# Kernel tuning notes

Hardware: AMD Instinct MI355X
Metric: run time of the kernel (lower is better)

## Reference

```python
import jax, jax.numpy as jnp
import numpy as np


def setup_inputs() -> dict:
    key = jax.random.key(0)
    k1, k2, k3 = jax.random.split(key, 3)
    B, C_in, H, W = 32, 128, 64, 64
    C_out, KH, KW = 256, 3, 3
    x = jax.random.normal(k1, (B, C_in, H, W), dtype=jnp.float32)
    # kaiming_normal fan_out scale ~ sqrt(2 / (C_out*KH*KW)); plain normal is fine for a numeric reference
    weight = jax.random.normal(k2, (C_out, C_in, KH, KW), dtype=jnp.float32) * (2.0 / (C_out * KH * KW)) ** 0.5
    fan_in = C_in * KH * KW
    bound = 1.0 / (fan_in ** 0.5)
    bias = jax.random.uniform(k3, (C_out,), dtype=jnp.float32, minval=-bound, maxval=bound)
    return {"x": x, "weight": weight, "bias": bias}


def reference(x, weight, bias):
    # Equivalent of unfold (im2col) + matmul + fold with stride=1, padding=1:
    # a standard 2D convolution in NCHW/OIHW layout.
    out = jax.lax.conv_general_dilated(
        x, weight,
        window_strides=(1, 1),
        padding=((1, 1), (1, 1)),
        dimension_numbers=("NCHW", "OIHW", "NCHW"),
    )
    return out + bias[None, :, None, None]
```

## Files before the change

### kernel.cpp

```cpp
#include <hip/hip_runtime.h>

typedef __attribute__((ext_vector_type(4))) int   v4i;
typedef __attribute__((ext_vector_type(8))) short s8;
typedef __attribute__((ext_vector_type(4))) float f32x4;
typedef __attribute__((ext_vector_type(16))) float f32x16;

#define GLB __attribute__((address_space(1)))
#define LDS_AS __attribute__((address_space(3)))

__device__ __forceinline__ unsigned short f2bf(float f) {
  unsigned u = __builtin_bit_cast(unsigned, f);
  return (unsigned short)((u + 0x7fffu + ((u >> 16) & 1u)) >> 16);
}

__global__ void prep(const float* __restrict__ x, const float* __restrict__ w,
                     unsigned int* __restrict__ xw, unsigned short* __restrict__ ww) {
  int t = threadIdx.x;
  if (blockIdx.x >= 2048) {
    int o = (blockIdx.x - 2048) * 256 + t;
    int tap = o >> 15;
    int c   = (o >> 13) & 3;
    int cog = (o >> 10) & 7;
    int kk  = (o >> 9) & 1;
    int lh  = (o >> 8) & 1;
    int l31 = (o >> 3) & 31;
    int e   = o & 7;
    int co = cog * 32 + l31;
    int ci = c * 32 + kk * 16 + lh * 8 + e;
    ww[o] = f2bf(w[(co * 128 + ci) * 9 + tap]);
    return;
  }
  __shared__ float tile[128][65];
  int bid = blockIdx.x;
  int b = bid >> 6, h = bid & 63;
  {
    int wcol = t & 63, cl = t >> 6;
    const float* src = x + ((size_t)(b * 128) * 64 + h) * 64 + wcol;
#pragma unroll
    for (int j = 0; j < 32; ++j) {
      int ci = j * 4 + cl;
      tile[ci][wcol] = src[(size_t)ci * 4096];
    }
  }
  unsigned int* dst = xw + (size_t)((b * 66 + h + 1) * 66) * 64;
  if (t < 128) {
    int col = (t >> 6) ? 65 : 0;
    dst[(size_t)col * 64 + (t & 63)] = 0u;
  }
  if (h == 0 || h == 63) {
    unsigned int* rb = xw + (size_t)(b * 66 + (h == 0 ? 0 : 65)) * 66 * 64;
    for (int j = t; j < 66 * 64; j += 256) rb[j] = 0u;
  }
  __syncthreads();
  {
    int ci2 = (t & 63) * 2, wl = t >> 6;
#pragma unroll
    for (int j = 0; j < 16; ++j) {
      int wcol = j * 4 + wl;
      unsigned p = (unsigned)f2bf(tile[ci2][wcol]) |
                   ((unsigned)f2bf(tile[ci2 + 1][wcol]) << 16);
      dst[(size_t)(wcol + 1) * 64 + (t & 63)] = p;
    }
  }
}

__global__ __launch_bounds__(256, 3) void conv_mfma(
    const unsigned short* __restrict__ xw, const unsigned short* __restrict__ ww,
    const float* __restrict__ bias, float* __restrict__ out) {
  __shared__ unsigned short Xl[204 * 128];
  const int tid = threadIdx.x;
  const int lane = tid & 63;
  const int l31 = lane & 31, lh = lane >> 5;
  const int mw = tid >> 6;
  int bid = blockIdx.x;
  bid = (bid & 7) * 256 + (bid >> 3);
  const int b = bid >> 6, h0 = bid & 63;
  const unsigned xlb = (unsigned)(unsigned long long)((LDS_AS void*)Xl);

  {
    const char* xbase = (const char*)xw;
#pragma unroll
    for (int it = 0; it < 13; ++it) {
      int s = tid + it * 256;
      if (s < 3264) {
        int q = s >> 4, p = s & 15;
        int u = p ^ (q & 15);
        int rr = q / 68, cc = q - rr * 68;
        if (cc > 65) cc = 65;
        unsigned src = (unsigned)((b * 66 + h0 + rr) * 66 + cc) * 256u + (unsigned)u * 16u;
        __builtin_amdgcn_global_load_lds((const GLB unsigned int*)(xbase + src),
                                         (LDS_AS unsigned int*)&Xl[s * 8], 16, 0, 0);
      }
    }
  }

  f32x16 acc[2][2];
#pragma unroll
  for (int m = 0; m < 2; ++m)
#pragma unroll
    for (int n = 0; n < 2; ++n)
#pragma unroll
      for (int e = 0; e < 16; ++e) acc[m][n][e] = 0.f;

  v4i areg[3][4];
  v4i breg[2][4];
  const unsigned abyte = (unsigned)(mw * 4096 + lane * 16);

  #define SB __builtin_amdgcn_sched_barrier(0)

  #define ALOAD_ASM(slot, step)                                               \
    do {                                                                      \
      unsigned _wo = (unsigned)(step) * 16384u + abyte;                       \
      asm volatile("global_load_dwordx4 %0, %1, %2 offset:0"                  \
                   : "=v"(areg[slot][0]) : "v"(_wo), "s"(ww));                \
      asm volatile("global_load_dwordx4 %0, %1, %2 offset:1024"               \
                   : "=v"(areg[slot][1]) : "v"(_wo), "s"(ww));                \
      asm volatile("global_load_dwordx4 %0, %1, %2 offset:2048"               \
                   : "=v"(areg[slot][2]) : "v"(_wo), "s"(ww));                \
      asm volatile("global_load_dwordx4 %0, %1, %2 offset:3072"               \
                   : "=v"(areg[slot][3]) : "v"(_wo), "s"(ww));                \
    } while (0)

  #define BLOAD_K0(slot, S)                                                   \
    do {                                                                      \
      const int _t = (S) >> 2, _c = (S) & 3;                                  \
      const int _kh = _t / 3, _kw = _t - _kh * 3;                             \
      const int _q0 = _kh * 68 + _kw + l31;                                   \
      const int _xq = (_q0 & 15) ^ lh;                                        \
      unsigned _a0 = xlb + (unsigned)((_q0 << 8) + (((_c * 4) ^ _xq) << 4));  \
      asm volatile("ds_read_b128 %0, %1" : "=v"(breg[slot][0]) : "v"(_a0));   \
      asm volatile("ds_read_b128 %0, %1 offset:8192"                          \
                   : "=v"(breg[slot][1]) : "v"(_a0));                         \
    } while (0)

  #define BLOAD_K1(slot, S)                                                   \
    do {                                                                      \
      const int _t = (S) >> 2, _c = (S) & 3;                                  \
      const int _kh = _t / 3, _kw = _t - _kh * 3;                             \
      const int _q0 = _kh * 68 + _kw + l31;                                   \
      const int _xq = (_q0 & 15) ^ lh;                                        \
      unsigned _a1 = xlb + (unsigned)((_q0 << 8) + (((_c * 4 + 2) ^ _xq) << 4)); \
      asm volatile("ds_read_b128 %0, %1" : "=v"(breg[slot][2]) : "v"(_a1));   \
      asm volatile("ds_read_b128 %0, %1 offset:8192"                          \
                   : "=v"(breg[slot][3]) : "v"(_a1));                         \
    } while (0)

  #define MFMA(d, af, bf) \
    d = __builtin_amdgcn_mfma_f32_32x32x16_bf16(__builtin_bit_cast(s8, af), \
                                                __builtin_bit_cast(s8, bf), d, 0, 0, 0)

  #define KSTEP(S)                                                            \
    do {                                                                      \
      const int _s = (S);                                                     \
      const int _cs = _s % 3, _bs = _s & 1, _ns = (_s + 1) & 1;               \
      if (_s < 35) asm volatile("s_waitcnt vmcnt(4) lgkmcnt(0)" ::: "memory");\
      else         asm volatile("s_waitcnt vmcnt(0) lgkmcnt(0)" ::: "memory");\
      SB;                                                                     \
      MFMA(acc[0][0], areg[_cs][0], breg[_bs][0]);                            \
      MFMA(acc[1][0], areg[_cs][2], breg[_bs][0]);                            \
      SB;                                                                     \
      if (_s < 34) ALOAD_ASM((_s + 2) % 3, _s + 2);                           \
      SB;                                                                     \
      MFMA(acc[0][1], areg[_cs][0], breg[_bs][1]);                            \
      MFMA(acc[1][1], areg[_cs][2], breg[_bs][1]);                            \
      SB;                                                                     \
      if (_s < 35) BLOAD_K0(_ns, _s + 1);                                     \
      SB;                                                                     \
      MFMA(acc[0][0], areg[_cs][1], breg[_bs][2]);                            \
      MFMA(acc[1][0], areg[_cs][3], breg[_bs][2]);                            \
      SB;                                                                     \
      if (_s < 35) BLOAD_K1(_ns, _s + 1);                                     \
      SB;                                                                     \
      MFMA(acc[0][1], areg[_cs][1], breg[_bs][3]);                            \
      MFMA(acc[1][1], areg[_cs][3], breg[_bs][3]);                            \
    } while (0)

  ALOAD_ASM(0, 0);
  ALOAD_ASM(1, 1);
  asm volatile("s_waitcnt vmcnt(8)" ::: "memory");
  SB;
  __builtin_amdgcn_s_barrier();
  BLOAD_K0(0, 0);
  BLOAD_K1(0, 0);

#pragma unroll
  for (int s = 0; s < 36; ++s) KSTEP(s);

#pragma unroll
  for (int m = 0; m < 2; ++m)
#pragma unroll
    for (int rq = 0; rq < 4; ++rq) {
      const int cob = mw * 64 + m * 32 + 8 * rq + 4 * lh;
      const f32x4 bi = *(const f32x4*)(bias + cob);
#pragma unroll
      for (int n = 0; n < 2; ++n) {
        const int wc = n * 32 + l31;
        size_t base = ((size_t)(b * 256 + cob) * 64 + h0) * 64 + wc;
#pragma unroll
        for (int e = 0; e < 4; ++e)
          out[base + (size_t)e * 4096] = acc[m][n][rq * 4 + e] + bi[e];
      }
    }
}

__global__ void conv_naive(const float* __restrict__ x, const float* __restrict__ w,
                           const float* __restrict__ bias, float* __restrict__ out) {
  int i = blockIdx.x * 256 + threadIdx.x;
  int wc = i & 63, h = (i >> 6) & 63, co = (i >> 12) & 255, b = i >> 20;
  float s = bias[co];
  for (int ci = 0; ci < 128; ++ci)
#pragma unroll
    for (int kh = 0; kh < 3; ++kh) {
      int hh = h + kh - 1;
      if ((unsigned)hh >= 64u) continue;
#pragma unroll
      for (int kw = 0; kw < 3; ++kw) {
        int wg = wc + kw - 1;
        if ((unsigned)wg >= 64u) continue;
        s += x[((b * 128 + ci) * 64 + hh) * 64 + wg] *
             w[((co * 128 + ci) * 3 + kh) * 3 + kw];
      }
    }
  out[i] = s;
}

extern "C" void kernel_launch(void* const* d_in, const int* in_sizes, int n_in,
                              void* d_out, int out_size, void* d_ws, size_t ws_size,
                              hipStream_t stream) {
  const float* x    = (const float*)d_in[0];
  const float* w    = (const float*)d_in[1];
  const float* bias = (const float*)d_in[2];
  float* out = (float*)d_out;

  const size_t X_OFF  = 1ull << 20;
  const size_t XBYTES = 32ull * 66 * 66 * 128 * 2;
  const size_t NEED   = X_OFF + XBYTES;

  if (ws_size >= NEED) {
    unsigned short* ww = (unsigned short*)d_ws;
    unsigned short* xq = (unsigned short*)((char*)d_ws + X_OFF);
    hipLaunchKernelGGL(prep, dim3(3200), dim3(256), 0, stream, x, w,
                       (unsigned int*)xq, ww);
    hipLaunchKernelGGL(conv_mfma, dim3(2048), dim3(256), 0, stream, xq, ww, bias, out);
  } else {
    hipLaunchKernelGGL(conv_naive, dim3(131072), dim3(256), 0, stream, x, w, bias, out);
  }
}
```

Before: 102.7 us.

## Compute two output rows per block to reuse weight fragments across rows

Each block now produces two output rows instead of one, staging four input rows in LDS and doubling the accumulators. Every weight fragment loaded from global memory feeds MFMAs for both rows, which halves weight traffic and the grid size. The K-step pipeline is reorganised into double-buffered A loads with grouped MFMA bursts. The cost is higher register and LDS use, which lowers occupancy from three to two blocks per CU, and fewer blocks to spread across CUs.

Measured after the change: 102.4 us. Within noise of the previous version (-0.3%).

```diff
diff --git a/kernel.cpp b/kernel.cpp
--- a/kernel.cpp
+++ b/kernel.cpp
@@ -64,29 +64,28 @@
   }
 }
 
-__global__ __launch_bounds__(256, 3) void conv_mfma(
+__global__ __launch_bounds__(256, 2) void conv_mfma(
     const unsigned short* __restrict__ xw, const unsigned short* __restrict__ ww,
     const float* __restrict__ bias, float* __restrict__ out) {
-  __shared__ unsigned short Xl[204 * 128];
+  __shared__ unsigned short Xl[264 * 128];
   const int tid = threadIdx.x;
   const int lane = tid & 63;
   const int l31 = lane & 31, lh = lane >> 5;
   const int mw = tid >> 6;
   int bid = blockIdx.x;
-  bid = (bid & 7) * 256 + (bid >> 3);
-  const int b = bid >> 6, h0 = bid & 63;
+  bid = (bid & 7) * 128 + (bid >> 3);
+  const int b = bid >> 5, h0 = (bid & 31) << 1;
   const unsigned xlb = (unsigned)(unsigned long long)((LDS_AS void*)Xl);
 
   {
     const char* xbase = (const char*)xw;
 #pragma unroll
-    for (int it = 0; it < 13; ++it) {
+    for (int it = 0; it < 17; ++it) {
       int s = tid + it * 256;
-      if (s < 3264) {
+      if (s < 4224) {
         int q = s >> 4, p = s & 15;
         int u = p ^ (q & 15);
-        int rr = q / 68, cc = q - rr * 68;
-        if (cc > 65) cc = 65;
+        int rr = q / 66, cc = q - rr * 66;
         unsigned src = (unsigned)((b * 66 + h0 + rr) * 66 + cc) * 256u + (unsigned)u * 16u;
         __builtin_amdgcn_global_load_lds((const GLB unsigned int*)(xbase + src),
                                          (LDS_AS unsigned int*)&Xl[s * 8], 16, 0, 0);
@@ -94,16 +93,17 @@
     }
   }
 
-  f32x16 acc[2][2];
+  f32x16 acc[2][4];
 #pragma unroll
   for (int m = 0; m < 2; ++m)
 #pragma unroll
-    for (int n = 0; n < 2; ++n)
+    for (int n = 0; n < 4; ++n)
 #pragma unroll
       for (int e = 0; e < 16; ++e) acc[m][n][e] = 0.f;
 
-  v4i areg[3][4];
+  v4i areg[2][4];
   v4i breg[2][4];
+  v4i bregB[4];
   const unsigned abyte = (unsigned)(mw * 4096 + lane * 16);
 
   #define SB __builtin_amdgcn_sched_barrier(0)
@@ -121,28 +121,36 @@
                    : "=v"(areg[slot][3]) : "v"(_wo), "s"(ww));                \
     } while (0)
 
-  #define BLOAD_K0(slot, S)                                                   \
+  #define BLOAD01(slot, S)                                                    \
     do {                                                                      \
       const int _t = (S) >> 2, _c = (S) & 3;                                  \
       const int _kh = _t / 3, _kw = _t - _kh * 3;                             \
-      const int _q0 = _kh * 68 + _kw + l31;                                   \
-      const int _xq = (_q0 & 15) ^ lh;                                        \
-      unsigned _a0 = xlb + (unsigned)((_q0 << 8) + (((_c * 4) ^ _xq) << 4));  \
+      const int _q = _kh * 66 + _kw + l31;                                    \
+      const int _x = (_q & 15) ^ lh;                                          \
+      unsigned _a0 = xlb + (unsigned)((_q << 8) + (((_c * 4) ^ _x) << 4));    \
+      unsigned _a1 = xlb + (unsigned)((_q << 8) + (((_c * 4 + 2) ^ _x) << 4));\
       asm volatile("ds_read_b128 %0, %1" : "=v"(breg[slot][0]) : "v"(_a0));   \
       asm volatile("ds_read_b128 %0, %1 offset:8192"                          \
                    : "=v"(breg[slot][1]) : "v"(_a0));                         \
-    } while (0)
-
-  #define BLOAD_K1(slot, S)                                                   \
+      asm volatile("ds_read_b128 %0, %1" : "=v"(breg[slot][2]) : "v"(_a1));   \
+      asm volatile("ds_read_b128 %0, %1 offset:8192"                          \
+                   : "=v"(breg[slot][3]) : "v"(_a1));                         \
+    } while (0)
+
+  #define BLOADB23(S)                                                         \
     do {                                                                      \
       const int _t = (S) >> 2, _c = (S) & 3;                                  \
       const int _kh = _t / 3, _kw = _t - _kh * 3;                             \
-      const int _q0 = _kh * 68 + _kw + l31;                                   \
-      const int _xq = (_q0 & 15) ^ lh;                                        \
-      unsigned _a1 = xlb + (unsigned)((_q0 << 8) + (((_c * 4 + 2) ^ _xq) << 4)); \
-      asm volatile("ds_read_b128 %0, %1" : "=v"(breg[slot][2]) : "v"(_a1));   \
-      asm volatile("ds_read_b128 %0, %1 offset:8192"                          \
-                   : "=v"(breg[slot][3]) : "v"(_a1));                         \
+      const int _q = (_kh + 1) * 66 + _kw + l31;                              \
+      const int _x = (_q & 15) ^ lh;                                          \
+      unsigned _a0 = xlb + (unsigned)((_q << 8) + (((_c * 4) ^ _x) << 4));    \
+      unsigned _a1 = xlb + (unsigned)((_q << 8) + (((_c * 4 + 2) ^ _x) << 4));\
+      asm volatile("ds_read_b128 %0, %1" : "=v"(bregB[0]) : "v"(_a0));        \
+      asm volatile("ds_read_b128 %0, %1 offset:8192"                          \
+                   : "=v"(bregB[1]) : "v"(_a0));                              \
+      asm volatile("ds_read_b128 %0, %1" : "=v"(bregB[2]) : "v"(_a1));        \
+      asm volatile("ds_read_b128 %0, %1 offset:8192"                          \
+                   : "=v"(bregB[3]) : "v"(_a1));                              \
     } while (0)
 
   #define MFMA(d, af, bf) \
@@ -152,36 +160,46 @@
   #define KSTEP(S)                                                            \
     do {                                                                      \
       const int _s = (S);                                                     \
-      const int _cs = _s % 3, _bs = _s & 1, _ns = (_s + 1) & 1;               \
-      if (_s < 35) asm volatile("s_waitcnt vmcnt(4) lgkmcnt(0)" ::: "memory");\
-      else         asm volatile("s_waitcnt vmcnt(0) lgkmcnt(0)" ::: "memory");\
+      const int _cs = _s & 1, _ns = (_s + 1) & 1;                             \
+      BLOADB23(_s);                                                           \
+      if (_s < 35) {                                                          \
+        ALOAD_ASM(_ns, _s + 1);                                               \
+        asm volatile("s_waitcnt vmcnt(4) lgkmcnt(4)" ::: "memory");           \
+      } else {                                                                \
+        asm volatile("s_waitcnt vmcnt(0) lgkmcnt(4)" ::: "memory");           \
+      }                                                                       \
       SB;                                                                     \
-      MFMA(acc[0][0], areg[_cs][0], breg[_bs][0]);                            \
-      MFMA(acc[1][0], areg[_cs][2], breg[_bs][0]);                            \
+      MFMA(acc[0][0], areg[_cs][0], breg[_cs][0]);                            \
+      MFMA(acc[1][0], areg[_cs][2], breg[_cs][0]);                            \
+      MFMA(acc[0][1], areg[_cs][0], breg[_cs][1]);                            \
+      MFMA(acc[1][1], areg[_cs][2], breg[_cs][1]);                            \
+      MFMA(acc[0][0], areg[_cs][1], breg[_cs][2]);                            \
+      MFMA(acc[1][0], areg[_cs][3], breg[_cs][2]);                            \
+      MFMA(acc[0][1], areg[_cs][1], breg[_cs][3]);                            \
+      MFMA(acc[1][1], areg[_cs][3], breg[_cs][3]);                            \
       SB;                                                                     \
-      if (_s < 34) ALOAD_ASM((_s + 2) % 3, _s + 2);                           \
+      if (_s < 35) {                                                          \
+        BLOAD01(_ns, _s + 1);                                                 \
+        asm volatile("s_waitcnt lgkmcnt(4)" ::: "memory");                    \
+      } else {                                                                \
+        asm volatile("s_waitcnt lgkmcnt(0)" ::: "memory");                    \
+      }                                                                       \
       SB;                                                                     \
-      MFMA(acc[0][1], areg[_cs][0], breg[_bs][1]);                            \
-      MFMA(acc[1][1], areg[_cs][2], breg[_bs][1]);                            \
-      SB;                                                                     \
-      if (_s < 35) BLOAD_K0(_ns, _s + 1);                                     \
-      SB;                                                                     \
-      MFMA(acc[0][0], areg[_cs][1], breg[_bs][2]);                            \
-      MFMA(acc[1][0], areg[_cs][3], breg[_bs][2]);                            \
-      SB;                                                                     \
-      if (_s < 35) BLOAD_K1(_ns, _s + 1);                                     \
-      SB;                                                                     \
-      MFMA(acc[0][1], areg[_cs][1], breg[_bs][3]);                            \
-      MFMA(acc[1][1], areg[_cs][3], breg[_bs][3]);                            \
+      MFMA(acc[0][2], areg[_cs][0], bregB[0]);                                \
+      MFMA(acc[1][2], areg[_cs][2], bregB[0]);                                \
+      MFMA(acc[0][3], areg[_cs][0], bregB[1]);                                \
+      MFMA(acc[1][3], areg[_cs][2], bregB[1]);                                \
+      MFMA(acc[0][2], areg[_cs][1], bregB[2]);                                \
+      MFMA(acc[1][2], areg[_cs][3], bregB[2]);                                \
+      MFMA(acc[0][3], areg[_cs][1], bregB[3]);                                \
+      MFMA(acc[1][3], areg[_cs][3], bregB[3]);                                \
     } while (0)
 
   ALOAD_ASM(0, 0);
-  ALOAD_ASM(1, 1);
-  asm volatile("s_waitcnt vmcnt(8)" ::: "memory");
+  asm volatile("s_waitcnt vmcnt(4)" ::: "memory");
   SB;
   __builtin_amdgcn_s_barrier();
-  BLOAD_K0(0, 0);
-  BLOAD_K1(0, 0);
+  BLOAD01(0, 0);
 
 #pragma unroll
   for (int s = 0; s < 36; ++s) KSTEP(s);
@@ -193,9 +211,9 @@
       const int cob = mw * 64 + m * 32 + 8 * rq + 4 * lh;
       const f32x4 bi = *(const f32x4*)(bias + cob);
 #pragma unroll
-      for (int n = 0; n < 2; ++n) {
-        const int wc = n * 32 + l31;
-        size_t base = ((size_t)(b * 256 + cob) * 64 + h0) * 64 + wc;
+      for (int n = 0; n < 4; ++n) {
+        const int row = h0 + (n >> 1), wc = (n & 1) * 32 + l31;
+        size_t base = ((size_t)(b * 256 + cob) * 64 + row) * 64 + wc;
 #pragma unroll
         for (int e = 0; e < 4; ++e)
           out[base + (size_t)e * 4096] = acc[m][n][rq * 4 + e] + bi[e];
@@ -241,7 +259,7 @@
     unsigned short* xq = (unsigned short*)((char*)d_ws + X_OFF);
     hipLaunchKernelGGL(prep, dim3(3200), dim3(256), 0, stream, x, w,
                        (unsigned int*)xq, ww);
-    hipLaunchKernelGGL(conv_mfma, dim3(2048), dim3(256), 0, stream, xq, ww, bias, out);
+    hipLaunchKernelGGL(conv_mfma, dim3(1024), dim3(256), 0, stream, xq, ww, bias, out);
   } else {
     hipLaunchKernelGGL(conv_naive, dim3(131072), dim3(256), 0, stream, x, w, bias, out);
   }
```
